# Kernel optimization log

Measured on AMD Instinct MI355X. Metric: run time of the kernel, lower is better.

Reference implementation:

```python
import jax, jax.numpy as jnp
import numpy as np

CAP = 512  # per-expert capacity; mean tokens/expert = 4096*4/64 = 256, CAP = mean + ~16 sigma (no drops for seed 0)


def _moe_forward(hidden_states, gate_w, w13, w2, top_k):
    T, H = hidden_states.shape
    E = gate_w.shape[0]
    # --- gating: softmax over expert logits, then top-k (npu_moe_gating_top_k_softmax) ---
    logits = hidden_states @ gate_w.T                      # [T, E]
    probs = jax.nn.softmax(logits, axis=-1)
    topk_w, topk_idx = jax.lax.top_k(probs, top_k)         # [T, K]
    # norm_topk_prob=True and top_k > 1
    topk_w = topk_w / (topk_w.sum(axis=-1, keepdims=True) + 1e-20)
    # --- init_routing: compute each (token, slot)'s rank within its expert ---
    N = T * top_k
    flat_e = topk_idx.reshape(N)                           # [N] expert id per expanded row
    order = jnp.argsort(flat_e)                            # stable sort by expert
    sorted_e = flat_e[order]
    counts = jax.ops.segment_sum(jnp.ones((N,), jnp.int32), flat_e, num_segments=E)
    starts = jnp.cumsum(counts) - counts                   # [E] start offset of each expert group
    rank_sorted = jnp.arange(N, dtype=jnp.int32) - starts[sorted_e].astype(jnp.int32)
    rank = jnp.zeros((N,), jnp.int32).at[order].set(rank_sorted)  # within-expert position
    # --- dispatch into [E, CAP, H] buffers (token gather/scatter) ---
    x_rep = jnp.repeat(hidden_states, top_k, axis=0)       # [N, H]
    disp = jnp.zeros((E, CAP, H), hidden_states.dtype).at[flat_e, rank].set(x_rep)
    # --- grouped GEMM: SwiGLU expert FFN as batched matmuls ---
    h = jnp.einsum('ech,ehf->ecf', disp, w13)              # [E, CAP, 2I]
    g, u = jnp.split(h, 2, axis=-1)
    a = jax.nn.silu(g) * u                                 # [E, CAP, I]
    y = jnp.einsum('eci,eih->ech', a, w2)                  # [E, CAP, H]
    # --- finalize_routing: gather back and weighted combine ---
    out_rows = y[flat_e, rank]                             # [N, H]
    out = (out_rows.reshape(T, top_k, H) * topk_w[..., None]).sum(axis=1)
    return out


def setup_inputs() -> dict:
    key = jax.random.key(0)
    k1, k2, k3, k4 = jax.random.split(key, 4)
    T, H, E, I = 4096, 2048, 64, 768
    hidden_states = jax.random.normal(k1, (T, H), dtype=jnp.float32)
    gate_w = jax.random.normal(k2, (E, H), dtype=jnp.float32) * 0.02
    w13 = jax.random.normal(k3, (E, H, 2 * I), dtype=jnp.float32) * 0.02
    w2 = jax.random.normal(k4, (E, I, H), dtype=jnp.float32) * 0.02
    return {"hidden_states": hidden_states, "gate_w": gate_w, "w13": w13, "w2": w2, "top_k": 4}


def reference(hidden_states, gate_w, w13, w2, top_k):
    return _moe_forward(hidden_states, gate_w, w13, w2, top_k)
```

## Files before the change

kernel.cpp:

```cpp
#include <hip/hip_runtime.h>
#include <hip/hip_bf16.h>

#define T_TOK 4096
#define HDIM  2048
#define NEXP  64
#define IDIM  768
#define TOPK  4
#define CAPE  512
#define NFLAT (T_TOK*TOPK)

typedef __bf16        bf16x8 __attribute__((ext_vector_type(8)));
typedef float         f32x4  __attribute__((ext_vector_type(4)));
typedef unsigned int  u32x4  __attribute__((ext_vector_type(4)));

__device__ __forceinline__ unsigned short f2bf(float f) {
  unsigned u = __builtin_bit_cast(unsigned, f);
  u = u + 0x7FFFu + ((u >> 16) & 1u);
  return (unsigned short)(u >> 16);
}
__device__ __forceinline__ unsigned pack2(float lo, float hi) {
  return (unsigned)f2bf(lo) | ((unsigned)f2bf(hi) << 16);
}

__global__ __launch_bounds__(256) void k_gating(
    const float* __restrict__ hs, const float* __restrict__ gw,
    unsigned short* __restrict__ hs_bf, int* __restrict__ tidx, float* __restrict__ tw)
{
  __shared__ float lg[16][64];
  const int tid = threadIdx.x;
  const int t0  = blockIdx.x * 16;

  {
    const f32x4* src = (const f32x4*)(hs + (size_t)t0 * HDIM);
    for (int i = tid; i < 16 * HDIM / 4; i += 256) {
      f32x4 v = src[i];
      ushort4 o;
      o.x = f2bf(v[0]); o.y = f2bf(v[1]); o.z = f2bf(v[2]); o.w = f2bf(v[3]);
      *(ushort4*)(hs_bf + (size_t)t0 * HDIM + (size_t)i * 4) = o;
    }
  }

  const int lane = tid & 63, wv = tid >> 6;
  {
    const f32x4* gr = (const f32x4*)(gw + (size_t)lane * HDIM);
    const f32x4* x0 = (const f32x4*)(hs + (size_t)(t0 + wv*4 + 0) * HDIM);
    const f32x4* x1 = (const f32x4*)(hs + (size_t)(t0 + wv*4 + 1) * HDIM);
    const f32x4* x2 = (const f32x4*)(hs + (size_t)(t0 + wv*4 + 2) * HDIM);
    const f32x4* x3 = (const f32x4*)(hs + (size_t)(t0 + wv*4 + 3) * HDIM);
    float a0=0.f, a1=0.f, a2=0.f, a3=0.f;
    for (int h = 0; h < HDIM/4; ++h) {
      f32x4 g = gr[h];
      f32x4 v0 = x0[h], v1 = x1[h], v2 = x2[h], v3 = x3[h];
      a0 += g[0]*v0[0] + g[1]*v0[1] + g[2]*v0[2] + g[3]*v0[3];
      a1 += g[0]*v1[0] + g[1]*v1[1] + g[2]*v1[2] + g[3]*v1[3];
      a2 += g[0]*v2[0] + g[1]*v2[1] + g[2]*v2[2] + g[3]*v2[3];
      a3 += g[0]*v3[0] + g[1]*v3[1] + g[2]*v3[2] + g[3]*v3[3];
    }
    lg[wv*4+0][lane] = a0;
    lg[wv*4+1][lane] = a1;
    lg[wv*4+2][lane] = a2;
    lg[wv*4+3][lane] = a3;
  }
  __syncthreads();

  if (tid < 16) {
    const int t = t0 + tid;
    unsigned long long chosen = 0ull;
    float bv[4]; int bi[4];
#pragma unroll
    for (int k = 0; k < 4; ++k) {
      float best = -1e30f; int b = 0;
      for (int e = 0; e < 64; ++e) {
        float v = lg[tid][e];
        if (!((chosen >> e) & 1ull) && v > best) { best = v; b = e; }
      }
      chosen |= 1ull << b; bv[k] = best; bi[k] = b;
    }
    float s = 0.f, w[4];
#pragma unroll
    for (int k = 0; k < 4; ++k) { w[k] = __expf(bv[k] - bv[0]); s += w[k]; }
    float inv = 1.f / s;
#pragma unroll
    for (int k = 0; k < 4; ++k) { tidx[t*4+k] = bi[k]; tw[t*4+k] = w[k] * inv; }
  }
}

__global__ __launch_bounds__(64) void k_count_rank(
    const int* __restrict__ tidx, int* __restrict__ rankb, int* __restrict__ counts)
{
  const int e = blockIdx.x;
  const int lane = threadIdx.x;
  int base = 0;
  for (int c = 0; c < NFLAT/64; ++c) {
    int n = c*64 + lane;
    bool m = (tidx[n] == e);
    unsigned long long mask = __ballot(m);
    if (m) rankb[n] = base + __popcll(mask & ((1ull << lane) - 1ull));
    base += __popcll(mask);
  }
  if (lane == 0) counts[e] = base;
}

__global__ __launch_bounds__(256) void k_build(
    const int* __restrict__ tidx, const float* __restrict__ tw,
    const int* __restrict__ rankb, const int* __restrict__ counts,
    int* __restrict__ starts, int* __restrict__ row_info, float* __restrict__ w_row)
{
  __shared__ int s_starts[NEXP];
  if (threadIdx.x == 0) {
    int s = 0;
    for (int e = 0; e < NEXP; ++e) { s_starts[e] = s; starts[e] = s; s += counts[e]; }
  }
  __syncthreads();
  for (int n = threadIdx.x; n < NFLAT; n += 256) {
    int e = tidx[n], r = rankb[n];
    int sr = s_starts[e] + r;
    row_info[sr] = n;
    w_row[sr]   = (r < CAPE) ? tw[n] : 0.f;
  }
}

__global__ __launch_bounds__(256, 2) void k_gemm1(
    const unsigned short* __restrict__ hs_bf, const float* __restrict__ w13,
    const int* __restrict__ counts, const int* __restrict__ starts,
    const int* __restrict__ row_info, unsigned short* __restrict__ a_buf)
{
  const int nt = blockIdx.x;
  const int mt = blockIdx.y;
  const int e  = blockIdx.z;
  const int count = min(counts[e], CAPE);
  const int R0 = mt * 128;
  if (R0 >= count) return;
  const int tid = threadIdx.x;
  const int base_sorted = starts[e] + R0;

  __shared__ __align__(16) char lds[3*16384];
  char* Alds = lds;
  char* Bgl  = lds + 16384;
  char* Bul  = lds + 32768;

  const int mrow = tid >> 3, cchunk = tid & 7;
  int tokp[4];
#pragma unroll
  for (int p = 0; p < 4; ++p) {
    int sr = base_sorted + mrow + p*32;
    if (sr > NFLAT-1) sr = NFLAT-1;
    tokp[p] = row_info[sr] >> 2;
  }
  const float* w13e = w13 + (size_t)e * HDIM * (2*IDIM);
  const int kg = tid >> 5;
  const int n4 = (tid & 31) * 4;

  const int lane = tid & 63, wv = tid >> 6;
  const int wr = wv >> 1, wc = wv & 1;

  f32x4 accg[4][4], accu[4][4];
#pragma unroll
  for (int i = 0; i < 4; ++i)
#pragma unroll
    for (int j = 0; j < 4; ++j) { accg[i][j] = f32x4{0.f,0.f,0.f,0.f}; accu[i][j] = f32x4{0.f,0.f,0.f,0.f}; }

  for (int kt = 0; kt < HDIM/64; ++kt) {
#pragma unroll
    for (int p = 0; p < 4; ++p) {
      int m = mrow + p*32;
      u32x4 v = *(const u32x4*)(hs_bf + (size_t)tokp[p]*HDIM + kt*64 + cchunk*8);
      *(u32x4*)(Alds + m*128 + ((cchunk ^ (m & 7)) << 4)) = v;
    }
#pragma unroll
    for (int half = 0; half < 2; ++half) {
      const float* bp = w13e + (size_t)(kt*64 + kg*8) * (2*IDIM) + half*IDIM + nt*128 + n4;
      f32x4 f[8];
#pragma unroll
      for (int j = 0; j < 8; ++j) f[j] = *(const f32x4*)(bp + (size_t)j * (2*IDIM));
      char* Bl = half ? Bul : Bgl;
#pragma unroll
      for (int i = 0; i < 4; ++i) {
        int n = n4 + i;
        u32x4 q;
        q[0] = pack2(f[0][i], f[1][i]);
        q[1] = pack2(f[2][i], f[3][i]);
        q[2] = pack2(f[4][i], f[5][i]);
        q[3] = pack2(f[6][i], f[7][i]);
        *(u32x4*)(Bl + n*128 + ((kg ^ (n & 7)) << 4)) = q;
      }
    }
    __syncthreads();
#pragma unroll
    for (int kfi = 0; kfi < 2; ++kfi) {
      bf16x8 af[4], bg[4], bu[4];
#pragma unroll
      for (int mi = 0; mi < 4; ++mi) {
        int row = wr*64 + mi*16 + (lane & 15);
        af[mi] = *(const bf16x8*)(Alds + row*128 + ((((kfi<<2)|(lane>>4)) ^ (row & 7)) << 4));
      }
#pragma unroll
      for (int ni = 0; ni < 4; ++ni) {
        int n = wc*64 + ni*16 + (lane & 15);
        int c = (((kfi<<2)|(lane>>4)) ^ (n & 7)) << 4;
        bg[ni] = *(const bf16x8*)(Bgl + n*128 + c);
        bu[ni] = *(const bf16x8*)(Bul + n*128 + c);
      }
#pragma unroll
      for (int mi = 0; mi < 4; ++mi)
#pragma unroll
        for (int ni = 0; ni < 4; ++ni) {
          accg[mi][ni] = __builtin_amdgcn_mfma_f32_16x16x32_bf16(af[mi], bg[ni], accg[mi][ni], 0, 0, 0);
          accu[mi][ni] = __builtin_amdgcn_mfma_f32_16x16x32_bf16(af[mi], bu[ni], accu[mi][ni], 0, 0, 0);
        }
    }
    __syncthreads();
  }

#pragma unroll
  for (int mi = 0; mi < 4; ++mi) {
#pragma unroll
    for (int j = 0; j < 4; ++j) {
      int rl = wr*64 + mi*16 + (lane >> 4)*4 + j;
      if (R0 + rl < count) {
        size_t rowoff = (size_t)(base_sorted + rl) * IDIM;
#pragma unroll
        for (int ni = 0; ni < 4; ++ni) {
          int col = nt*128 + wc*64 + ni*16 + (lane & 15);
          float g = accg[mi][ni][j], u = accu[mi][ni][j];
          float a = (g / (1.f + __expf(-g))) * u;
          a_buf[rowoff + col] = f2bf(a);
        }
      }
    }
  }
}

__global__ __launch_bounds__(256, 2) void k_gemm2(
    const unsigned short* __restrict__ a_buf, const float* __restrict__ w2,
    const int* __restrict__ counts, const int* __restrict__ starts,
    const int* __restrict__ row_info, const float* __restrict__ w_row,
    float* __restrict__ out)
{
  const int nt = blockIdx.x;
  const int mt = blockIdx.y;
  const int e  = blockIdx.z;
  const int count = min(counts[e], CAPE);
  const int R0 = mt * 128;
  if (R0 >= count) return;
  const int tid = threadIdx.x;
  const int base_sorted = starts[e] + R0;

  __shared__ __align__(16) char lds[16384 + 32768];
  char* Alds = lds;
  char* Blds = lds + 16384;

  const int mrow = tid >> 3, cchunk = tid & 7;
  int srp[4];
#pragma unroll
  for (int p = 0; p < 4; ++p) {
    int sr = base_sorted + mrow + p*32;
    srp[p] = (sr > NFLAT-1) ? (NFLAT-1) : sr;
  }
  const float* w2e = w2 + (size_t)e * IDIM * HDIM;
  const int kg = tid >> 5, n4 = (tid & 31) * 4;
  const int lane = tid & 63, wv = tid >> 6, wr = wv >> 1, wc = wv & 1;

  f32x4 acc[4][8];
#pragma unroll
  for (int i = 0; i < 4; ++i)
#pragma unroll
    for (int j = 0; j < 8; ++j) acc[i][j] = f32x4{0.f,0.f,0.f,0.f};

  for (int kt = 0; kt < IDIM/64; ++kt) {
#pragma unroll
    for (int p = 0; p < 4; ++p) {
      int m = mrow + p*32;
      u32x4 v = *(const u32x4*)(a_buf + (size_t)srp[p]*IDIM + kt*64 + cchunk*8);
      *(u32x4*)(Alds + m*128 + ((cchunk ^ (m & 7)) << 4)) = v;
    }
#pragma unroll
    for (int pass = 0; pass < 2; ++pass) {
      int nn = n4 + pass*128;
      const float* bp = w2e + (size_t)(kt*64 + kg*8) * HDIM + nt*256 + nn;
      f32x4 f[8];
#pragma unroll
      for (int j = 0; j < 8; ++j) f[j] = *(const f32x4*)(bp + (size_t)j * HDIM);
#pragma unroll
      for (int i = 0; i < 4; ++i) {
        int n = nn + i;
        u32x4 q;
        q[0] = pack2(f[0][i], f[1][i]);
        q[1] = pack2(f[2][i], f[3][i]);
        q[2] = pack2(f[4][i], f[5][i]);
        q[3] = pack2(f[6][i], f[7][i]);
        *(u32x4*)(Blds + n*128 + ((kg ^ (n & 7)) << 4)) = q;
      }
    }
    __syncthreads();
#pragma unroll
    for (int kfi = 0; kfi < 2; ++kfi) {
      bf16x8 af[4], bb[8];
#pragma unroll
      for (int mi = 0; mi < 4; ++mi) {
        int row = wr*64 + mi*16 + (lane & 15);
        af[mi] = *(const bf16x8*)(Alds + row*128 + ((((kfi<<2)|(lane>>4)) ^ (row & 7)) << 4));
      }
#pragma unroll
      for (int ni = 0; ni < 8; ++ni) {
        int n = wc*128 + ni*16 + (lane & 15);
        bb[ni] = *(const bf16x8*)(Blds + n*128 + (((((kfi<<2)|(lane>>4)) ^ (n & 7))) << 4));
      }
#pragma unroll
      for (int mi = 0; mi < 4; ++mi)
#pragma unroll
        for (int ni = 0; ni < 8; ++ni)
          acc[mi][ni] = __builtin_amdgcn_mfma_f32_16x16x32_bf16(af[mi], bb[ni], acc[mi][ni], 0, 0, 0);
    }
    __syncthreads();
  }

#pragma unroll
  for (int mi = 0; mi < 4; ++mi) {
#pragma unroll
    for (int j = 0; j < 4; ++j) {
      int rl = wr*64 + mi*16 + (lane >> 4)*4 + j;
      if (R0 + rl < count) {
        int sr = base_sorted + rl;
        int info = row_info[sr];
        int t = info >> 2;
        float wgt = w_row[sr];
        float* orow = out + (size_t)t * HDIM;
#pragma unroll
        for (int ni = 0; ni < 8; ++ni) {
          int col = nt*256 + wc*128 + ni*16 + (lane & 15);
          atomicAdd(orow + col, wgt * acc[mi][ni][j]);
        }
      }
    }
  }
}

extern "C" void kernel_launch(void* const* d_in, const int* in_sizes, int n_in,
                              void* d_out, int out_size, void* d_ws, size_t ws_size,
                              hipStream_t stream) {
  const float* hs  = (const float*)d_in[0];
  const float* gw  = (const float*)d_in[1];
  const float* w13 = (const float*)d_in[2];
  const float* w2  = (const float*)d_in[3];
  float* out = (float*)d_out;

  char* ws = (char*)d_ws;
  size_t off = 0;
  auto alloc = [&](size_t bytes) {
    off = (off + 255) & ~(size_t)255;
    char* p = ws + off;
    off += bytes;
    return p;
  };
  unsigned short* hs_bf = (unsigned short*)alloc((size_t)T_TOK * HDIM * 2);
  int*   tidx   = (int*)  alloc((size_t)NFLAT * 4);
  float* tw     = (float*)alloc((size_t)NFLAT * 4);
  int*   rankb  = (int*)  alloc((size_t)NFLAT * 4);
  int*   counts = (int*)  alloc((size_t)NEXP * 4);
  int*   starts = (int*)  alloc((size_t)NEXP * 4);
  int*   rinfo  = (int*)  alloc((size_t)NFLAT * 4);
  float* wrow   = (float*)alloc((size_t)NFLAT * 4);
  unsigned short* a_buf = (unsigned short*)alloc((size_t)NFLAT * IDIM * 2);
  (void)ws_size; (void)in_sizes; (void)n_in; (void)out_size;

  hipMemsetAsync(d_out, 0, (size_t)T_TOK * HDIM * 4, stream);
  k_gating<<<T_TOK/16, 256, 0, stream>>>(hs, gw, hs_bf, tidx, tw);
  k_count_rank<<<NEXP, 64, 0, stream>>>(tidx, rankb, counts);
  k_build<<<1, 256, 0, stream>>>(tidx, tw, rankb, counts, starts, rinfo, wrow);
  k_gemm1<<<dim3(6, 4, NEXP), 256, 0, stream>>>(hs_bf, w13, counts, starts, rinfo, a_buf);
  k_gemm2<<<dim3(8, 4, NEXP), 256, 0, stream>>>(a_buf, w2, counts, starts, rinfo, wrow, out);
}
```

Baseline: 935.0 us.

## Replace atomic scatter-add in down-proj GEMM with sorted y buffer and finalize kernel

The second GEMM now writes its per-row results in plain stores to a sorted fp32 y buffer instead of doing weighted atomicAdds into the output. A new per-token finalize kernel gathers the four expert rows, weights them and writes the output with vector stores. This also removes the output memset. It is meant to eliminate atomic contention and scattered read-modify-write traffic, at the cost of an extra 128MB write plus read of the intermediate buffer and one more launch.

```diff
diff --git a/kernel.cpp b/kernel.cpp
--- a/kernel.cpp
+++ b/kernel.cpp
@@ -102,9 +102,9 @@
 }
 
 __global__ __launch_bounds__(256) void k_build(
-    const int* __restrict__ tidx, const float* __restrict__ tw,
-    const int* __restrict__ rankb, const int* __restrict__ counts,
-    int* __restrict__ starts, int* __restrict__ row_info, float* __restrict__ w_row)
+    const int* __restrict__ tidx, const int* __restrict__ rankb,
+    const int* __restrict__ counts,
+    int* __restrict__ starts, int* __restrict__ row_info, int* __restrict__ sortpos)
 {
   __shared__ int s_starts[NEXP];
   if (threadIdx.x == 0) {
@@ -116,7 +116,7 @@
     int e = tidx[n], r = rankb[n];
     int sr = s_starts[e] + r;
     row_info[sr] = n;
-    w_row[sr]   = (r < CAPE) ? tw[n] : 0.f;
+    sortpos[n] = (r < CAPE) ? sr : -1;
   }
 }
 
@@ -234,8 +234,7 @@
 __global__ __launch_bounds__(256, 2) void k_gemm2(
     const unsigned short* __restrict__ a_buf, const float* __restrict__ w2,
     const int* __restrict__ counts, const int* __restrict__ starts,
-    const int* __restrict__ row_info, const float* __restrict__ w_row,
-    float* __restrict__ out)
+    float* __restrict__ y_buf)
 {
   const int nt = blockIdx.x;
   const int mt = blockIdx.y;
@@ -322,18 +321,37 @@
       int rl = wr*64 + mi*16 + (lane >> 4)*4 + j;
       if (R0 + rl < count) {
         int sr = base_sorted + rl;
-        int info = row_info[sr];
-        int t = info >> 2;
-        float wgt = w_row[sr];
-        float* orow = out + (size_t)t * HDIM;
+        float* yrow = y_buf + (size_t)sr * HDIM;
 #pragma unroll
         for (int ni = 0; ni < 8; ++ni) {
           int col = nt*256 + wc*128 + ni*16 + (lane & 15);
-          atomicAdd(orow + col, wgt * acc[mi][ni][j]);
+          yrow[col] = acc[mi][ni][j];
         }
       }
     }
   }
+}
+
+__global__ __launch_bounds__(256) void k_finalize(
+    const float* __restrict__ y_buf, const int* __restrict__ sortpos,
+    const float* __restrict__ tw, float* __restrict__ out)
+{
+  const int t = blockIdx.x;
+  const int tid = threadIdx.x;
+  f32x4 acc0 = {0.f,0.f,0.f,0.f}, acc1 = {0.f,0.f,0.f,0.f};
+#pragma unroll
+  for (int k = 0; k < 4; ++k) {
+    int sp = sortpos[t*4+k];
+    float w = tw[t*4+k];
+    if (sp >= 0) {
+      const f32x4* yr = (const f32x4*)(y_buf + (size_t)sp * HDIM);
+      acc0 += w * yr[tid];
+      acc1 += w * yr[tid + 256];
+    }
+  }
+  f32x4* o = (f32x4*)(out + (size_t)t * HDIM);
+  o[tid] = acc0;
+  o[tid + 256] = acc1;
 }
 
 extern "C" void kernel_launch(void* const* d_in, const int* in_sizes, int n_in,
@@ -360,14 +378,15 @@
   int*   counts = (int*)  alloc((size_t)NEXP * 4);
   int*   starts = (int*)  alloc((size_t)NEXP * 4);
   int*   rinfo  = (int*)  alloc((size_t)NFLAT * 4);
-  float* wrow   = (float*)alloc((size_t)NFLAT * 4);
+  int*   sortp  = (int*)  alloc((size_t)NFLAT * 4);
   unsigned short* a_buf = (unsigned short*)alloc((size_t)NFLAT * IDIM * 2);
+  float* y_buf  = (float*)alloc((size_t)NFLAT * HDIM * 4);
   (void)ws_size; (void)in_sizes; (void)n_in; (void)out_size;
 
-  hipMemsetAsync(d_out, 0, (size_t)T_TOK * HDIM * 4, stream);
   k_gating<<<T_TOK/16, 256, 0, stream>>>(hs, gw, hs_bf, tidx, tw);
   k_count_rank<<<NEXP, 64, 0, stream>>>(tidx, rankb, counts);
-  k_build<<<1, 256, 0, stream>>>(tidx, tw, rankb, counts, starts, rinfo, wrow);
+  k_build<<<1, 256, 0, stream>>>(tidx, rankb, counts, starts, rinfo, sortp);
   k_gemm1<<<dim3(6, 4, NEXP), 256, 0, stream>>>(hs_bf, w13, counts, starts, rinfo, a_buf);
-  k_gemm2<<<dim3(8, 4, NEXP), 256, 0, stream>>>(a_buf, w2, counts, starts, rinfo, wrow, out);
-}
+  k_gemm2<<<dim3(8, 4, NEXP), 256, 0, stream>>>(a_buf, w2, counts, starts, y_buf);
+  k_finalize<<<T_TOK, 256, 0, stream>>>(y_buf, sortp, tw, out);
+}
```

Result: faster. 866.3 us (-7.4%).
